# Kernel optimization log

Measured on AMD Instinct MI355X. Metric: run time of the kernel, lower is better.

## Reference

```python
import jax, jax.numpy as jnp
import numpy as np

HIDDEN = 1024
HEADS = 16
HEAD_DIM = HIDDEN // HEADS


def setup_inputs() -> dict:
    key = jax.random.key(0)
    k1, k2, k3, k4, k5 = jax.random.split(key, 5)
    x = jax.random.normal(k1, (2, 4096, HIDDEN), dtype=jnp.float32)
    # torch nn.Linear params: weight [out, in], bias [out]
    s = 1.0 / np.sqrt(HIDDEN)
    qkv_w = jax.random.uniform(k2, (3 * HIDDEN, HIDDEN), jnp.float32, -s, s)
    qkv_b = jax.random.uniform(k3, (3 * HIDDEN,), jnp.float32, -s, s)
    out_w = jax.random.uniform(k4, (HIDDEN, HIDDEN), jnp.float32, -s, s)
    out_b = jax.random.uniform(k5, (HIDDEN,), jnp.float32, -s, s)
    return {"x": x, "qkv_w": qkv_w, "qkv_b": qkv_b, "out_w": out_w, "out_b": out_b}


def reference(x, qkv_w, qkv_b, out_w, out_b):
    B, N, C = x.shape
    qkv = x @ qkv_w.T + qkv_b  # [B, N, 3C]
    qkv = qkv.reshape(B, N, 3, HEADS, HEAD_DIM)
    qkv = jnp.transpose(qkv, (2, 0, 3, 1, 4))  # [3, B, H, N, D]
    q, k, v = qkv[0], qkv[1], qkv[2]
    scale = HEAD_DIM ** -0.5
    attn = jnp.einsum('bhnd,bhmd->bhnm', q, k) * scale
    attn = jax.nn.softmax(attn, axis=-1)
    out = jnp.einsum('bhnm,bhmd->bhnd', attn, v)  # [B, H, N, D]
    out = jnp.transpose(out, (0, 2, 1, 3)).reshape(B, N, C)
    return out @ out_w.T + out_b
```

## Files before the change

kernel.cpp:

```cpp
#include <hip/hip_runtime.h>
#include <hip/hip_bf16.h>

using bf16 = __hip_bfloat16;
typedef __attribute__((ext_vector_type(8))) short short8;
typedef __attribute__((ext_vector_type(4))) short short4v;
typedef __attribute__((ext_vector_type(4))) float floatx4;

#define MFMA16(a, b, c) __builtin_amdgcn_mfma_f32_16x16x32_bf16((a), (b), (c), 0, 0, 0)

constexpr int HID = 1024;
constexpr int NH = 16;
constexpr int HD = 64;
constexpr int NB = 2;
constexpr int SEQL = 4096;
#define QPRE 0.18033688011112042f

__device__ __forceinline__ short f32_to_bf16_bits(float p) {
    bf16 b = __float2bfloat16(p);
    short s;
    __builtin_memcpy(&s, &b, sizeof(s));
    return s;
}

__device__ __forceinline__ short8 cvt8(floatx4 a, floatx4 b) {
    short8 r;
#pragma unroll
    for (int i = 0; i < 4; ++i) {
        r[i]     = f32_to_bf16_bits(a[i]);
        r[i + 4] = f32_to_bf16_bits(b[i]);
    }
    return r;
}

__device__ __forceinline__ void gld16(const void* g, void* l) {
    __builtin_amdgcn_global_load_lds(
        (const __attribute__((address_space(1))) void*)g,
        (__attribute__((address_space(3))) void*)l, 16, 0, 0);
}


__global__ __launch_bounds__(256)
void cvt_pack(float* __restrict__ p, int n8)
{
    const int i = blockIdx.x * 256 + threadIdx.x;
    if (i < n8) {
        const floatx4 a = ((const floatx4*)p)[2 * i];
        const floatx4 b = ((const floatx4*)p)[2 * i + 1];
        ((short8*)p)[2 * i] = cvt8(a, b);
    }
}

template <int MODE>
__global__ __launch_bounds__(256)
void gemm_bt(const char* __restrict__ A_, const char* __restrict__ W,
             const float* __restrict__ bias, void* __restrict__ out0_,
             bf16* __restrict__ out1, bf16* __restrict__ out2)
{
    __shared__ __align__(16) short As[128 * 64];
    __shared__ __align__(16) short Bs[128 * 64];
    const int tid  = threadIdx.x;
    const int wave = tid >> 6;
    const int lane = tid & 63;
    const int quad = lane >> 4;
    const int l16  = lane & 15;
    const int sw   = l16 & 7;
    const int wm   = wave >> 1;
    const int wn   = wave & 1;
    const int m0   = blockIdx.y * 128;
    const int n0   = blockIdx.x * 128;
    const int lr   = lane >> 3;
    const int lcs  = (lane & 7) ^ (lr & 7);

    const size_t aElemB = (MODE == 1) ? 4 : 2;
    const char* ag = A_ + ((size_t)(m0 + wave * 32 + lr) * HID + lcs * 8) * aElemB;
    const char* bg = W  + ((size_t)(n0 + wave * 32 + lr) * HID + lcs * 8) * 4;
    const size_t aRow8 = (size_t)HID * 8 * aElemB;
    const size_t bRow8 = (size_t)HID * 8 * 4;
    short* asw = As + (wave * 32) * 64;
    short* bsw = Bs + (wave * 32) * 64;

    floatx4 acc[4][4];
#pragma unroll
    for (int i = 0; i < 4; ++i)
#pragma unroll
        for (int j = 0; j < 4; ++j)
            acc[i][j] = (floatx4){0.f, 0.f, 0.f, 0.f};

    for (int k0 = 0; k0 < HID; k0 += 64) {
        __syncthreads();
#pragma unroll
        for (int i = 0; i < 4; ++i) {
            gld16(ag + (size_t)i * aRow8 + (size_t)k0 * aElemB, asw + i * 8 * 64);
            gld16(bg + (size_t)i * bRow8 + (size_t)k0 * 4,      bsw + i * 8 * 64);
        }
        __syncthreads();
#pragma unroll
        for (int kk = 0; kk < 2; ++kk) {
            short8 af[4], bfr[4];
#pragma unroll
            for (int i = 0; i < 4; ++i) {
                af[i]  = *(const short8*)(As + (wm * 64 + i * 16 + l16) * 64 +
                                          (((kk * 4 + quad) ^ sw) * 8));
                bfr[i] = *(const short8*)(Bs + (wn * 64 + i * 16 + l16) * 64 +
                                          (((kk * 4 + quad) ^ sw) * 8));
            }
#pragma unroll
            for (int i = 0; i < 4; ++i)
#pragma unroll
                for (int j = 0; j < 4; ++j)
                    acc[i][j] = MFMA16(af[i], bfr[j], acc[i][j]);
        }
    }

#pragma unroll
    for (int j = 0; j < 4; ++j) {
        const int col = n0 + wn * 64 + j * 16 + l16;
        const float bv = bias[col];
        const int part = col >> 10;
        const int c = col & (HID - 1);
        const int h = c >> 6;
        const int d = c & 63;
#pragma unroll
        for (int i = 0; i < 4; ++i) {
            const int row0 = m0 + wm * 64 + i * 16 + quad * 4;
            if (MODE == 1 && part == 2) {
                const int b = row0 >> 12;
                const int npos0 = row0 & (SEQL - 1);
                short4v pk;
#pragma unroll
                for (int r = 0; r < 4; ++r)
                    pk[r] = f32_to_bf16_bits(acc[i][j][r] + bv);
                *(short4v*)(out2 + ((size_t)(b * NH + h) * HD + d) * SEQL + npos0) = pk;
            } else {
#pragma unroll
                for (int r = 0; r < 4; ++r) {
                    const int row = row0 + r;
                    const float v = acc[i][j][r] + bv;
                    if (MODE == 0) {
                        ((float*)out0_)[(size_t)row * HID + col] = v;
                    } else {
                        const int b = row >> 12;
                        const int npos = row & (SEQL - 1);
                        const size_t bh = (size_t)(b * NH + h);
                        if (part == 0)
                            ((bf16*)out0_)[(bh * SEQL + npos) * HD + d] =
                                __float2bfloat16(v * QPRE);
                        else
                            out1[(bh * SEQL + npos) * HD + d] = __float2bfloat16(v);
                    }
                }
            }
        }
    }
}

__global__ __launch_bounds__(512)
void flash_attn(const bf16* __restrict__ Qbf, const bf16* __restrict__ Kbf,
                const bf16* __restrict__ Vtbf, bf16* __restrict__ Og)
{
    __shared__ __align__(16) short Ks[64 * 64];
    __shared__ __align__(16) short Vs[64 * 64];
    __shared__ __align__(16) short Ps[256 * 72];
    const short* Qg = (const short*)Qbf;
    const int tid  = threadIdx.x;
    const int wave = tid >> 6;
    const int lane = tid & 63;
    const int quad = lane >> 4;
    const int l16  = lane & 15;
    const int sw   = l16 & 7;
    const int lr   = lane >> 3;
    const int lcs  = (lane & 7) ^ lr;
    const int bh   = blockIdx.y;
    const int q0   = blockIdx.x * 256;
    const size_t base = (size_t)bh * SEQL * HD;

    short8 qf[2][2];
#pragma unroll
    for (int mt = 0; mt < 2; ++mt) {
        const short* qp = Qg + base + (size_t)(q0 + wave * 32 + mt * 16 + l16) * HD + quad * 8;
        qf[mt][0] = *(const short8*)(qp);
        qf[mt][1] = *(const short8*)(qp + 32);
    }

    const char* kg = (const char*)Kbf + (base + (size_t)(wave * 8 + lr) * HD + lcs * 8) * 2;
    const char* vg = (const char*)Vtbf + (base + (size_t)(wave * 8 + lr) * SEQL + lcs * 8) * 2;
    short* ksw = Ks + (wave * 8) * 64;
    short* vsw = Vs + (wave * 8) * 64;

    floatx4 oacc[2][4];
    floatx4 lacc[2];
#pragma unroll
    for (int mt = 0; mt < 2; ++mt) {
        lacc[mt] = (floatx4){0.f, 0.f, 0.f, 0.f};
#pragma unroll
        for (int dt = 0; dt < 4; ++dt) oacc[mt][dt] = (floatx4){0.f, 0.f, 0.f, 0.f};
    }

    const short8 ONESF = (short8)(short)0x3F80;

    for (int kt = 0; kt < SEQL / 64; ++kt) {
        const int key0 = kt * 64;
        __syncthreads();
        gld16(kg + (size_t)key0 * HD * 2, ksw);
        gld16(vg + (size_t)key0 * 2,      vsw);
        __syncthreads();

        short8 kf[2][4];
#pragma unroll
        for (int n = 0; n < 4; ++n) {
            kf[0][n] = *(const short8*)(Ks + (n * 16 + l16) * 64 + ((quad ^ sw) * 8));
            kf[1][n] = *(const short8*)(Ks + (n * 16 + l16) * 64 + (((4 + quad) ^ sw) * 8));
        }

#pragma unroll
        for (int mt = 0; mt < 2; ++mt) {
            floatx4 s[4];
#pragma unroll
            for (int n = 0; n < 4; ++n) {
                s[n] = (floatx4){0.f, 0.f, 0.f, 0.f};
                s[n] = MFMA16(qf[mt][0], kf[0][n], s[n]);
                s[n] = MFMA16(qf[mt][1], kf[1][n], s[n]);
            }
            const int prow = (wave * 32 + mt * 16 + quad * 4) * 72 + l16;
#pragma unroll
            for (int n = 0; n < 4; ++n) {
#pragma unroll
                for (int r = 0; r < 4; ++r) {
                    const float p = __builtin_amdgcn_exp2f(s[n][r]);
                    Ps[prow + r * 72 + n * 16] = f32_to_bf16_bits(p);
                }
            }
        }

        short8 vf[2][4];
#pragma unroll
        for (int dt = 0; dt < 4; ++dt) {
            vf[0][dt] = *(const short8*)(Vs + (dt * 16 + l16) * 64 + ((quad ^ sw) * 8));
            vf[1][dt] = *(const short8*)(Vs + (dt * 16 + l16) * 64 + (((4 + quad) ^ sw) * 8));
        }

#pragma unroll
        for (int mt = 0; mt < 2; ++mt) {
            const short* pb = Ps + (wave * 32 + mt * 16 + l16) * 72 + quad * 8;
            short8 pf0 = *(const short8*)(pb);
            short8 pf1 = *(const short8*)(pb + 32);
#pragma unroll
            for (int dt = 0; dt < 4; ++dt) {
                oacc[mt][dt] = MFMA16(pf0, vf[0][dt], oacc[mt][dt]);
                oacc[mt][dt] = MFMA16(pf1, vf[1][dt], oacc[mt][dt]);
            }
            lacc[mt] = MFMA16(pf0, ONESF, lacc[mt]);
            lacc[mt] = MFMA16(pf1, ONESF, lacc[mt]);
        }
    }

    const int b = bh >> 4;
    const int h = bh & 15;
#pragma unroll
    for (int mt = 0; mt < 2; ++mt) {
        floatx4 inv;
#pragma unroll
        for (int r = 0; r < 4; ++r) inv[r] = 1.0f / lacc[mt][r];
#pragma unroll
        for (int dt = 0; dt < 4; ++dt) {
#pragma unroll
            for (int r = 0; r < 4; ++r) {
                const int npos = q0 + wave * 32 + mt * 16 + quad * 4 + r;
                const int col = h * HD + dt * 16 + l16;
                Og[((size_t)(b * SEQL + npos)) * HID + col] =
                    __float2bfloat16(oacc[mt][dt][r] * inv[r]);
            }
        }
    }
}

extern "C" void kernel_launch(void* const* d_in, const int* in_sizes, int n_in,
                              void* d_out, int out_size, void* d_ws, size_t ws_size,
                              hipStream_t stream)
{
    float* x     = (float*)d_in[0];
    float* qkv_w = (float*)d_in[1];
    const float* qkv_b = (const float*)d_in[2];
    float* out_w = (float*)d_in[3];
    const float* out_b = (const float*)d_in[4];
    float* out = (float*)d_out;

    const size_t SZ = (size_t)NB * NH * SEQL * HD;
    bf16* q_ws  = (bf16*)d_ws;
    bf16* k_ws  = q_ws + SZ;
    bf16* vt_ws = k_ws + SZ;
    bf16* a_ws  = vt_ws + SZ;

    dim3 blk(256);
    cvt_pack<<<dim3((NB * SEQL * HID) / 8 / 256), blk, 0, stream>>>(x, NB * SEQL * HID / 8);
    cvt_pack<<<dim3((3 * HID * HID) / 8 / 256), blk, 0, stream>>>(qkv_w, 3 * HID * HID / 8);
    cvt_pack<<<dim3((HID * HID) / 8 / 256), blk, 0, stream>>>(out_w, HID * HID / 8);

    gemm_bt<1><<<dim3(3 * HID / 128, NB * SEQL / 128), blk, 0, stream>>>(
        (const char*)x, (const char*)qkv_w, qkv_b, q_ws, k_ws, vt_ws);
    flash_attn<<<dim3(SEQL / 256, NB * NH), dim3(512), 0, stream>>>(q_ws, k_ws, vt_ws, a_ws);
    gemm_bt<0><<<dim3(HID / 128, NB * SEQL / 128), blk, 0, stream>>>(
        (const char*)a_ws, (const char*)out_w, out_b, out, nullptr, nullptr);
}
```

Before: 367.2 us.

## Double-buffer K/V tiles in LDS and raise wave priority around MFMAs

Splits the K and V shared-memory tiles into two buffers. The next key tile's global-to-LDS load is issued before computing on the current one, so load latency overlaps with the QK^T/exp/PV work. The loop is unrolled by two, which also removes one barrier per tile. s_setprio is raised around the MFMA blocks to favour matrix issue across waves. The cost is twice the LDS for K/V, which may affect occupancy.

```diff
diff --git a/kernel.cpp b/kernel.cpp
--- a/kernel.cpp
+++ b/kernel.cpp
@@ -158,8 +158,8 @@
 void flash_attn(const bf16* __restrict__ Qbf, const bf16* __restrict__ Kbf,
                 const bf16* __restrict__ Vtbf, bf16* __restrict__ Og)
 {
-    __shared__ __align__(16) short Ks[64 * 64];
-    __shared__ __align__(16) short Vs[64 * 64];
+    __shared__ __align__(16) short Ks[2][64 * 64];
+    __shared__ __align__(16) short Vs[2][64 * 64];
     __shared__ __align__(16) short Ps[256 * 72];
     const short* Qg = (const short*)Qbf;
     const int tid  = threadIdx.x;
@@ -184,8 +184,10 @@
 
     const char* kg = (const char*)Kbf + (base + (size_t)(wave * 8 + lr) * HD + lcs * 8) * 2;
     const char* vg = (const char*)Vtbf + (base + (size_t)(wave * 8 + lr) * SEQL + lcs * 8) * 2;
-    short* ksw = Ks + (wave * 8) * 64;
-    short* vsw = Vs + (wave * 8) * 64;
+    short* ks0 = Ks[0] + (wave * 8) * 64;
+    short* ks1 = Ks[1] + (wave * 8) * 64;
+    short* vs0 = Vs[0] + (wave * 8) * 64;
+    short* vs1 = Vs[1] + (wave * 8) * 64;
 
     floatx4 oacc[2][4];
     floatx4 lacc[2];
@@ -198,29 +200,25 @@
 
     const short8 ONESF = (short8)(short)0x3F80;
 
-    for (int kt = 0; kt < SEQL / 64; ++kt) {
-        const int key0 = kt * 64;
-        __syncthreads();
-        gld16(kg + (size_t)key0 * HD * 2, ksw);
-        gld16(vg + (size_t)key0 * 2,      vsw);
-        __syncthreads();
-
+    auto compute = [&](const short* Kb, const short* Vb) {
         short8 kf[2][4];
 #pragma unroll
         for (int n = 0; n < 4; ++n) {
-            kf[0][n] = *(const short8*)(Ks + (n * 16 + l16) * 64 + ((quad ^ sw) * 8));
-            kf[1][n] = *(const short8*)(Ks + (n * 16 + l16) * 64 + (((4 + quad) ^ sw) * 8));
+            kf[0][n] = *(const short8*)(Kb + (n * 16 + l16) * 64 + ((quad ^ sw) * 8));
+            kf[1][n] = *(const short8*)(Kb + (n * 16 + l16) * 64 + (((4 + quad) ^ sw) * 8));
         }
 
 #pragma unroll
         for (int mt = 0; mt < 2; ++mt) {
             floatx4 s[4];
+            __builtin_amdgcn_s_setprio(1);
 #pragma unroll
             for (int n = 0; n < 4; ++n) {
                 s[n] = (floatx4){0.f, 0.f, 0.f, 0.f};
                 s[n] = MFMA16(qf[mt][0], kf[0][n], s[n]);
                 s[n] = MFMA16(qf[mt][1], kf[1][n], s[n]);
             }
+            __builtin_amdgcn_s_setprio(0);
             const int prow = (wave * 32 + mt * 16 + quad * 4) * 72 + l16;
 #pragma unroll
             for (int n = 0; n < 4; ++n) {
@@ -235,8 +233,8 @@
         short8 vf[2][4];
 #pragma unroll
         for (int dt = 0; dt < 4; ++dt) {
-            vf[0][dt] = *(const short8*)(Vs + (dt * 16 + l16) * 64 + ((quad ^ sw) * 8));
-            vf[1][dt] = *(const short8*)(Vs + (dt * 16 + l16) * 64 + (((4 + quad) ^ sw) * 8));
+            vf[0][dt] = *(const short8*)(Vb + (dt * 16 + l16) * 64 + ((quad ^ sw) * 8));
+            vf[1][dt] = *(const short8*)(Vb + (dt * 16 + l16) * 64 + (((4 + quad) ^ sw) * 8));
         }
 
 #pragma unroll
@@ -244,6 +242,7 @@
             const short* pb = Ps + (wave * 32 + mt * 16 + l16) * 72 + quad * 8;
             short8 pf0 = *(const short8*)(pb);
             short8 pf1 = *(const short8*)(pb + 32);
+            __builtin_amdgcn_s_setprio(1);
 #pragma unroll
             for (int dt = 0; dt < 4; ++dt) {
                 oacc[mt][dt] = MFMA16(pf0, vf[0][dt], oacc[mt][dt]);
@@ -251,7 +250,29 @@
             }
             lacc[mt] = MFMA16(pf0, ONESF, lacc[mt]);
             lacc[mt] = MFMA16(pf1, ONESF, lacc[mt]);
-        }
+            __builtin_amdgcn_s_setprio(0);
+        }
+    };
+
+    constexpr int NT = SEQL / 64;
+
+    gld16(kg, ks0);
+    gld16(vg, vs0);
+
+    for (int kt = 0; kt < NT; kt += 2) {
+        __syncthreads();
+        if (kt + 1 < NT) {
+            gld16(kg + (size_t)(kt + 1) * 64 * HD * 2, ks1);
+            gld16(vg + (size_t)(kt + 1) * 64 * 2,      vs1);
+        }
+        compute(Ks[0], Vs[0]);
+
+        __syncthreads();
+        if (kt + 2 < NT) {
+            gld16(kg + (size_t)(kt + 2) * 64 * HD * 2, ks0);
+            gld16(vg + (size_t)(kt + 2) * 64 * 2,      vs0);
+        }
+        if (kt + 1 < NT) compute(Ks[1], Vs[1]);
     }
 
     const int b = bh >> 4;
```

After: 401.7 us. +9.4%, slower.
